# Performance work log

Hardware: AMD Instinct MI355X
Metric: run time of the kernel (lower is better)

The kernel has to match this reference:

```python
import jax, jax.numpy as jnp
import numpy as np

DIM = 768
NUM_HEADS = 12
HEAD_DIM = DIM // NUM_HEADS
SCALE = HEAD_DIM ** -0.5


def setup_inputs() -> dict:
    key = jax.random.key(0)
    k_x, k_qkv, k_pw, k_pb = jax.random.split(key, 4)
    B, N = 2, 4096
    x = jax.random.normal(k_x, (B, N, DIM), dtype=jnp.float32)
    # Linear weights stored as [in, out] for x @ W
    w_qkv = jax.random.normal(k_qkv, (DIM, 3 * DIM), dtype=jnp.float32) * (DIM ** -0.5)
    w_proj = jax.random.normal(k_pw, (DIM, DIM), dtype=jnp.float32) * (DIM ** -0.5)
    b_proj = jax.random.normal(k_pb, (DIM,), dtype=jnp.float32) * 0.02
    return {"x": x, "w_qkv": w_qkv, "w_proj": w_proj, "b_proj": b_proj}


def reference(x, w_qkv, w_proj, b_proj):
    B, N, D = x.shape
    H, Hd = NUM_HEADS, HEAD_DIM
    qkv = (x @ w_qkv).reshape(B, N, 3, H, Hd)
    qkv = jnp.transpose(qkv, (2, 0, 3, 1, 4))  # [3, B, H, N, Hd]
    q, k, v = qkv[0], qkv[1], qkv[2]
    attn = jnp.einsum("bhnd,bhmd->bhnm", q, k) * SCALE  # [B,H,N,N]
    attn = jax.nn.softmax(attn, axis=-1)
    out = jnp.einsum("bhnm,bhmd->bhnd", attn, v)  # [B,H,N,Hd]
    out = jnp.transpose(out, (0, 2, 1, 3)).reshape(B, N, D)
    return out @ w_proj + b_proj
```

## Files before the change

kernel.cpp:

```cpp
#include <hip/hip_runtime.h>
#include <hip/hip_bf16.h>


#define NSEQ 4096
#define NTOK 8192
#define NHD  12
#define QSCALE 0.18033688011112043f

typedef __attribute__((ext_vector_type(8))) __bf16 bf16x8;
typedef __attribute__((ext_vector_type(4))) __bf16 bf16x4;
typedef __attribute__((ext_vector_type(8))) unsigned short u16x8;
typedef __attribute__((ext_vector_type(4))) float  f32x4;

typedef const __attribute__((address_space(1))) unsigned int* as1_u32p;
typedef __attribute__((address_space(3))) unsigned int*       as3_u32p;

#if defined(__has_builtin)
#  if __has_builtin(__builtin_amdgcn_exp2f)
#    define EXP2(x) __builtin_amdgcn_exp2f(x)
#  else
#    define EXP2(x) exp2f(x)
#  endif
#else
#  define EXP2(x) exp2f(x)
#endif

__device__ inline f32x4 mfma16(bf16x8 a, bf16x8 b, f32x4 c) {
    return __builtin_amdgcn_mfma_f32_16x16x32_bf16(a, b, c, 0, 0, 0);
}

__device__ __forceinline__ void gload16(const __bf16* g, __bf16* l) {
    __builtin_amdgcn_global_load_lds((as1_u32p)g, (as3_u32p)l, 16, 0, 0);
}

__global__ __launch_bounds__(256)
void cvt_bf16_kernel(const float* __restrict__ x, __bf16* __restrict__ y)
{
    const size_t i = ((size_t)blockIdx.x * 256 + threadIdx.x) * 8;
    f32x4 a = *(const f32x4*)(x + i);
    f32x4 b = *(const f32x4*)(x + i + 4);
    bf16x8 w;
    #pragma unroll
    for (int j = 0; j < 4; ++j) { w[j] = (__bf16)a[j]; w[4 + j] = (__bf16)b[j]; }
    *(bf16x8*)(y + i) = w;
}

__global__ __launch_bounds__(256)
void wT_kernel(const float* __restrict__ W, __bf16* __restrict__ WT, int K, int N)
{
    __shared__ float t[32][33];
    const int tid = threadIdx.x;
    const int bk = blockIdx.x * 32, bn = blockIdx.y * 32;
    const int tx = tid & 31, ty = tid >> 5;
    #pragma unroll
    for (int i = 0; i < 4; ++i)
        t[ty + 8 * i][tx] = W[(size_t)(bk + ty + 8 * i) * N + bn + tx];
    __syncthreads();
    const int n = bn + (tid >> 3), kc = (tid & 7) * 4;
    bf16x4 w;
    #pragma unroll
    for (int j = 0; j < 4; ++j) w[j] = (__bf16)t[kc + j][tid >> 3];
    *(bf16x4*)(WT + (size_t)n * K + bk + kc) = w;
}

template<int EPI>
__global__ __launch_bounds__(256)
void gemm_kernel(const __bf16* __restrict__ A, const __bf16* __restrict__ BT,
                 const float* __restrict__ bias, void* __restrict__ Cp,
                 int M, int N, int K)
{
    __shared__ __bf16 lds_a[128 * 32];
    __shared__ __bf16 lds_b[128 * 32];
    const int tid  = threadIdx.x;
    const int lane = tid & 63, wave = tid >> 6;
    const int l16  = lane & 15, lg = lane >> 4;
    const int wr = (wave >> 1) * 64, wc = (wave & 1) * 64;
    const int m0 = blockIdx.x * 128, n0 = blockIdx.y * 128;

    f32x4 acc[4][4] = {};

    for (int k0 = 0; k0 < K; k0 += 32) {
        #pragma unroll
        for (int i = 0; i < 2; ++i) {
            const int s   = i * 256 + tid;
            const int row = s >> 2, ch = s & 3;
            __bf16* la = lds_a + (i * 256 + wave * 64) * 8;
            __bf16* lb = lds_b + (i * 256 + wave * 64) * 8;
            gload16(A  + (size_t)(m0 + row) * K + k0 + ch * 8, la);
            gload16(BT + (size_t)(n0 + row) * K + k0 + ch * 8, lb);
        }
        __syncthreads();

        bf16x8 a[4], b[4];
        #pragma unroll
        for (int mf = 0; mf < 4; ++mf)
            a[mf] = *(const bf16x8*)&lds_a[(wr + mf * 16 + l16) * 32 + lg * 8];
        #pragma unroll
        for (int nf = 0; nf < 4; ++nf)
            b[nf] = *(const bf16x8*)&lds_b[(wc + nf * 16 + l16) * 32 + lg * 8];
        __builtin_amdgcn_s_setprio(1);
        #pragma unroll
        for (int mf = 0; mf < 4; ++mf)
            #pragma unroll
            for (int nf = 0; nf < 4; ++nf)
                acc[mf][nf] = mfma16(a[mf], b[nf], acc[mf][nf]);
        __builtin_amdgcn_s_setprio(0);
        __syncthreads();
    }

    #pragma unroll
    for (int mf = 0; mf < 4; ++mf) {
        #pragma unroll
        for (int nf = 0; nf < 4; ++nf) {
            int n = n0 + wc + nf * 16 + l16;
            #pragma unroll
            for (int r = 0; r < 4; ++r) {
                int m = m0 + wr + mf * 16 + lg * 4 + r;
                float v = acc[mf][nf][r];
                if constexpr (EPI == 0) {
                    if (n < 768) v *= QSCALE;
                    ((__bf16*)Cp)[(size_t)m * N + n] = (__bf16)v;
                } else {
                    ((float*)Cp)[(size_t)m * N + n] = v + bias[n];
                }
            }
        }
    }
}

__global__ __launch_bounds__(256)
void attn_kernel(const __bf16* __restrict__ qkv, __bf16* __restrict__ out)
{
    __shared__ __bf16 k_lds[2][64 * 72];
    __shared__ __bf16 v_lds[2][64 * 64];
    __shared__ __bf16 p_lds[4][32 * 72];

    const int tid = threadIdx.x, lane = tid & 63, wave = tid >> 6;
    const int l16 = lane & 15, lg = lane >> 4;

    int bid = (blockIdx.x & 7) * 96 + (blockIdx.x >> 3);
    const int qt = bid & 31;
    const int h  = (bid >> 5) % NHD;
    const int b  = bid / (32 * NHD);
    const size_t rowbase = (size_t)b * NSEQ;
    const int q0 = qt * 128 + wave * 32;

    bf16x8 qf[2][2];
    #pragma unroll
    for (int mf = 0; mf < 2; ++mf)
        #pragma unroll
        for (int ks = 0; ks < 2; ++ks)
            qf[mf][ks] = *(const bf16x8*)(qkv + (rowbase + q0 + mf * 16 + l16) * 2304
                                              + h * 64 + ks * 32 + lg * 8);

    f32x4 o[4][2] = {};
    float l_r[2] = {0.f, 0.f};

    const int krow = tid >> 3, kq = tid & 7;
    const int vt   = tid >> 3, vq = tid & 7;
    u16x8 kreg0, kreg1, vreg0, vreg1;

    auto load_kv = [&](int kt) {
        const unsigned short* q16 = (const unsigned short*)qkv;
        size_t base = rowbase + (size_t)kt * 64;
        kreg0 = *(const u16x8*)(q16 + (base + krow)        * 2304 + 768  + h * 64 + kq * 8);
        kreg1 = *(const u16x8*)(q16 + (base + krow + 32)   * 2304 + 768  + h * 64 + kq * 8);
        vreg0 = *(const u16x8*)(q16 + (base + 2 * vt)      * 2304 + 1536 + h * 64 + vq * 8);
        vreg1 = *(const u16x8*)(q16 + (base + 2 * vt + 1)  * 2304 + 1536 + h * 64 + vq * 8);
    };
    auto store_kv = [&](int bsel) {
        *(u16x8*)&k_lds[bsel][krow * 72 + kq * 8]        = kreg0;
        *(u16x8*)&k_lds[bsel][(krow + 32) * 72 + kq * 8] = kreg1;
        #pragma unroll
        for (int j = 0; j < 8; ++j) {
            int d = vq * 8 + j;
            int chunk = ((vt >> 2) ^ d ^ (d >> 3)) & 7;
            unsigned int val = (unsigned int)vreg0[j] | ((unsigned int)vreg1[j] << 16);
            *(unsigned int*)((char*)&v_lds[bsel][0] + d * 128 + chunk * 16 + (vt & 3) * 4) = val;
        }
    };

    load_kv(0);
    store_kv(0);
    __syncthreads();

    const int NT = NSEQ / 64;
    for (int kt = 0; kt < NT; ++kt) {
        const int cur = kt & 1;
        if (kt + 1 < NT) load_kv(kt + 1);

        f32x4 sc[4][2] = {};
        __builtin_amdgcn_s_setprio(1);
        #pragma unroll
        for (int tf = 0; tf < 4; ++tf) {
            #pragma unroll
            for (int ks = 0; ks < 2; ++ks) {
                bf16x8 kfr = *(const bf16x8*)&k_lds[cur][(tf * 16 + l16) * 72 + ks * 32 + lg * 8];
                #pragma unroll
                for (int mf = 0; mf < 2; ++mf)
                    sc[tf][mf] = mfma16(kfr, qf[mf][ks], sc[tf][mf]);
            }
        }
        __builtin_amdgcn_s_setprio(0);

        #pragma unroll
        for (int mf = 0; mf < 2; ++mf) {
            float rs = 0.f;
            #pragma unroll
            for (int tf = 0; tf < 4; ++tf)
                #pragma unroll
                for (int r = 0; r < 4; ++r) {
                    float p = EXP2(sc[tf][mf][r]);
                    sc[tf][mf][r] = p;
                    rs += p;
                }
            l_r[mf] += rs;
        }

        __bf16* pl = p_lds[wave];
        #pragma unroll
        for (int mf = 0; mf < 2; ++mf)
            #pragma unroll
            for (int tf = 0; tf < 4; ++tf) {
                bf16x4 w;
                #pragma unroll
                for (int r = 0; r < 4; ++r) w[r] = (__bf16)sc[tf][mf][r];
                *(bf16x4*)&pl[(mf * 16 + l16) * 72 + tf * 16 + lg * 4] = w;
            }
    asm volatile("s_waitcnt lgkmcnt(0)" ::: "memory");

        __builtin_amdgcn_s_setprio(1);
        #pragma unroll
        for (int ks = 0; ks < 2; ++ks) {
            bf16x8 pf[2];
            #pragma unroll
            for (int mf = 0; mf < 2; ++mf)
                pf[mf] = *(const bf16x8*)&pl[(mf * 16 + l16) * 72 + ks * 32 + lg * 8];
            #pragma unroll
            for (int nf = 0; nf < 4; ++nf) {
                int d = nf * 16 + l16;
                int chunk = ((ks * 4 + lg) ^ d ^ (d >> 3)) & 7;
                bf16x8 vf = *(const bf16x8*)((const char*)&v_lds[cur][0] + d * 128 + chunk * 16);
                #pragma unroll
                for (int mf = 0; mf < 2; ++mf)
                    o[nf][mf] = mfma16(vf, pf[mf], o[nf][mf]);
            }
        }
        __builtin_amdgcn_s_setprio(0);

        if (kt + 1 < NT) store_kv(cur ^ 1);
        __syncthreads();
    }

    #pragma unroll
    for (int mf = 0; mf < 2; ++mf) {
        l_r[mf] += __shfl_xor(l_r[mf], 16);
        l_r[mf] += __shfl_xor(l_r[mf], 32);
        float inv = 1.0f / l_r[mf];
        size_t row = rowbase + q0 + mf * 16 + l16;
        #pragma unroll
        for (int nf = 0; nf < 4; ++nf) {
            bf16x4 w;
            #pragma unroll
            for (int r = 0; r < 4; ++r) w[r] = (__bf16)(o[nf][mf][r] * inv);
            *(bf16x4*)(out + row * 768 + h * 64 + nf * 16 + lg * 4) = w;
        }
    }
}

extern "C" void kernel_launch(void* const* d_in, const int* in_sizes, int n_in,
                              void* d_out, int out_size, void* d_ws, size_t ws_size,
                              hipStream_t stream)
{
    const float* x      = (const float*)d_in[0];
    const float* w_qkv  = (const float*)d_in[1];
    const float* w_proj = (const float*)d_in[2];
    const float* b_proj = (const float*)d_in[3];
    float* out = (float*)d_out;

    __bf16* qkv    = (__bf16*)d_ws;
    __bf16* attn   = qkv + (size_t)NTOK * 2304;
    __bf16* wqkvT  = attn;
    __bf16* wprojT = attn + (size_t)NTOK * 768;
    __bf16* x_bf16 = (__bf16*)d_out;

    cvt_bf16_kernel<<<dim3(NTOK * 768 / (256 * 8)), 256, 0, stream>>>(x, x_bf16);
    wT_kernel<<<dim3(24, 72), 256, 0, stream>>>(w_qkv, wqkvT, 768, 2304);
    wT_kernel<<<dim3(24, 24), 256, 0, stream>>>(w_proj, wprojT, 768, 768);

    gemm_kernel<0><<<dim3(64, 18), 256, 0, stream>>>(x_bf16, wqkvT, nullptr, qkv,
                                                     NTOK, 3 * 768, 768);
    attn_kernel<<<dim3(2 * NHD * 32), 256, 0, stream>>>(qkv, attn);
    gemm_kernel<1><<<dim3(64, 6), 256, 0, stream>>>(attn, wprojT, b_proj, out,
                                                    NTOK, 768, 768);
}
```

Baseline: 316.5 us.

## Switch attention to 32x32x16 MFMA and keep P in registers via lane shuffles

Rewrites the attention inner loop to use 32x32x16 bf16 MFMA tiles instead of 16x16x32. Because of the new layout, the softmax probabilities can be packed and exchanged across half-waves with shuffles rather than written to and re-read from a per-wave LDS buffer. This removes the P LDS round trip and its wait, and issues fewer, larger MFMA instructions. It also sets an occupancy hint of 3 blocks per CU, which may constrain register allocation.

```diff
diff --git a/kernel.cpp b/kernel.cpp
--- a/kernel.cpp
+++ b/kernel.cpp
@@ -7,10 +7,12 @@
 #define NHD  12
 #define QSCALE 0.18033688011112043f
 
-typedef __attribute__((ext_vector_type(8))) __bf16 bf16x8;
-typedef __attribute__((ext_vector_type(4))) __bf16 bf16x4;
-typedef __attribute__((ext_vector_type(8))) unsigned short u16x8;
-typedef __attribute__((ext_vector_type(4))) float  f32x4;
+typedef __attribute__((ext_vector_type(8)))  __bf16 bf16x8;
+typedef __attribute__((ext_vector_type(4)))  __bf16 bf16x4;
+typedef __attribute__((ext_vector_type(2)))  __bf16 bf16x2;
+typedef __attribute__((ext_vector_type(8)))  unsigned short u16x8;
+typedef __attribute__((ext_vector_type(4)))  float  f32x4;
+typedef __attribute__((ext_vector_type(16))) float  f32x16;
 
 typedef const __attribute__((address_space(1))) unsigned int* as1_u32p;
 typedef __attribute__((address_space(3))) unsigned int*       as3_u32p;
@@ -28,6 +30,15 @@
 __device__ inline f32x4 mfma16(bf16x8 a, bf16x8 b, f32x4 c) {
     return __builtin_amdgcn_mfma_f32_16x16x32_bf16(a, b, c, 0, 0, 0);
 }
+__device__ inline f32x16 mfma32(bf16x8 a, bf16x8 b, f32x16 c) {
+    return __builtin_amdgcn_mfma_f32_32x32x16_bf16(a, b, c, 0, 0, 0);
+}
+
+__device__ inline unsigned int pack2(float x, float y) {
+    union { bf16x2 v; unsigned int u; } c;
+    c.v[0] = (__bf16)x; c.v[1] = (__bf16)y;
+    return c.u;
+}
 
 __device__ __forceinline__ void gload16(const __bf16* g, __bf16* l) {
     __builtin_amdgcn_global_load_lds((as1_u32p)g, (as3_u32p)l, 16, 0, 0);
@@ -128,33 +139,30 @@
     }
 }
 
-__global__ __launch_bounds__(256)
+__global__ __launch_bounds__(256, 3)
 void attn_kernel(const __bf16* __restrict__ qkv, __bf16* __restrict__ out)
 {
     __shared__ __bf16 k_lds[2][64 * 72];
     __shared__ __bf16 v_lds[2][64 * 64];
-    __shared__ __bf16 p_lds[4][32 * 72];
 
     const int tid = threadIdx.x, lane = tid & 63, wave = tid >> 6;
-    const int l16 = lane & 15, lg = lane >> 4;
+    const int l31 = lane & 31, hi = lane >> 5;
+    const bool hib = (hi != 0);
 
     int bid = (blockIdx.x & 7) * 96 + (blockIdx.x >> 3);
     const int qt = bid & 31;
     const int h  = (bid >> 5) % NHD;
     const int b  = bid / (32 * NHD);
     const size_t rowbase = (size_t)b * NSEQ;
-    const int q0 = qt * 128 + wave * 32;
-
-    bf16x8 qf[2][2];
-    #pragma unroll
-    for (int mf = 0; mf < 2; ++mf)
-        #pragma unroll
-        for (int ks = 0; ks < 2; ++ks)
-            qf[mf][ks] = *(const bf16x8*)(qkv + (rowbase + q0 + mf * 16 + l16) * 2304
-                                              + h * 64 + ks * 32 + lg * 8);
-
-    f32x4 o[4][2] = {};
-    float l_r[2] = {0.f, 0.f};
+    const int q = qt * 128 + wave * 32 + l31;
+
+    bf16x8 qf[4];
+    #pragma unroll
+    for (int ks = 0; ks < 4; ++ks)
+        qf[ks] = *(const bf16x8*)(qkv + (rowbase + q) * 2304 + h * 64 + ks * 16 + hi * 8);
+
+    f32x16 o[2] = {};
+    float l_r = 0.f;
 
     const int krow = tid >> 3, kq = tid & 7;
     const int vt   = tid >> 3, vq = tid & 7;
@@ -163,10 +171,10 @@
     auto load_kv = [&](int kt) {
         const unsigned short* q16 = (const unsigned short*)qkv;
         size_t base = rowbase + (size_t)kt * 64;
-        kreg0 = *(const u16x8*)(q16 + (base + krow)        * 2304 + 768  + h * 64 + kq * 8);
-        kreg1 = *(const u16x8*)(q16 + (base + krow + 32)   * 2304 + 768  + h * 64 + kq * 8);
-        vreg0 = *(const u16x8*)(q16 + (base + 2 * vt)      * 2304 + 1536 + h * 64 + vq * 8);
-        vreg1 = *(const u16x8*)(q16 + (base + 2 * vt + 1)  * 2304 + 1536 + h * 64 + vq * 8);
+        kreg0 = *(const u16x8*)(q16 + (base + krow)       * 2304 + 768  + h * 64 + kq * 8);
+        kreg1 = *(const u16x8*)(q16 + (base + krow + 32)  * 2304 + 768  + h * 64 + kq * 8);
+        vreg0 = *(const u16x8*)(q16 + (base + 2 * vt)     * 2304 + 1536 + h * 64 + vq * 8);
+        vreg1 = *(const u16x8*)(q16 + (base + 2 * vt + 1) * 2304 + 1536 + h * 64 + vq * 8);
     };
     auto store_kv = [&](int bsel) {
         *(u16x8*)&k_lds[bsel][krow * 72 + kq * 8]        = kreg0;
@@ -189,61 +197,56 @@
         const int cur = kt & 1;
         if (kt + 1 < NT) load_kv(kt + 1);
 
-        f32x4 sc[4][2] = {};
+        f32x16 sc[2] = {};
         __builtin_amdgcn_s_setprio(1);
         #pragma unroll
-        for (int tf = 0; tf < 4; ++tf) {
-            #pragma unroll
-            for (int ks = 0; ks < 2; ++ks) {
-                bf16x8 kfr = *(const bf16x8*)&k_lds[cur][(tf * 16 + l16) * 72 + ks * 32 + lg * 8];
-                #pragma unroll
-                for (int mf = 0; mf < 2; ++mf)
-                    sc[tf][mf] = mfma16(kfr, qf[mf][ks], sc[tf][mf]);
+        for (int tb = 0; tb < 2; ++tb) {
+            #pragma unroll
+            for (int ks = 0; ks < 4; ++ks) {
+                bf16x8 kf = *(const bf16x8*)&k_lds[cur][(tb * 32 + l31) * 72 + ks * 16 + hi * 8];
+                sc[tb] = mfma32(kf, qf[ks], sc[tb]);
             }
         }
         __builtin_amdgcn_s_setprio(0);
 
-        #pragma unroll
-        for (int mf = 0; mf < 2; ++mf) {
-            float rs = 0.f;
-            #pragma unroll
-            for (int tf = 0; tf < 4; ++tf)
-                #pragma unroll
-                for (int r = 0; r < 4; ++r) {
-                    float p = EXP2(sc[tf][mf][r]);
-                    sc[tf][mf][r] = p;
-                    rs += p;
-                }
-            l_r[mf] += rs;
-        }
-
-        __bf16* pl = p_lds[wave];
-        #pragma unroll
-        for (int mf = 0; mf < 2; ++mf)
-            #pragma unroll
-            for (int tf = 0; tf < 4; ++tf) {
-                bf16x4 w;
-                #pragma unroll
-                for (int r = 0; r < 4; ++r) w[r] = (__bf16)sc[tf][mf][r];
-                *(bf16x4*)&pl[(mf * 16 + l16) * 72 + tf * 16 + lg * 4] = w;
-            }
-    asm volatile("s_waitcnt lgkmcnt(0)" ::: "memory");
+        unsigned int pk0[2][4], pk1[2][4];
+        float rs = 0.f;
+        #pragma unroll
+        for (int tb = 0; tb < 2; ++tb) {
+            #pragma unroll
+            for (int g = 0; g < 4; ++g) {
+                float p0 = EXP2(sc[tb][4 * g + 0]);
+                float p1 = EXP2(sc[tb][4 * g + 1]);
+                float p2 = EXP2(sc[tb][4 * g + 2]);
+                float p3 = EXP2(sc[tb][4 * g + 3]);
+                rs += (p0 + p1) + (p2 + p3);
+                pk0[tb][g] = pack2(p0, p1);
+                pk1[tb][g] = pack2(p2, p3);
+            }
+        }
+        l_r += rs;
 
         __builtin_amdgcn_s_setprio(1);
         #pragma unroll
-        for (int ks = 0; ks < 2; ++ks) {
-            bf16x8 pf[2];
-            #pragma unroll
-            for (int mf = 0; mf < 2; ++mf)
-                pf[mf] = *(const bf16x8*)&pl[(mf * 16 + l16) * 72 + ks * 32 + lg * 8];
-            #pragma unroll
-            for (int nf = 0; nf < 4; ++nf) {
-                int d = nf * 16 + l16;
-                int chunk = ((ks * 4 + lg) ^ d ^ (d >> 3)) & 7;
+        for (int ks = 0; ks < 4; ++ks) {
+            const int tb = ks >> 1, gL = 2 * (ks & 1), gH = gL + 1;
+            unsigned int pL0 = pk0[tb][gL], pL1 = pk1[tb][gL];
+            unsigned int pH0 = pk0[tb][gH], pH1 = pk1[tb][gH];
+            unsigned int rL0 = (unsigned int)__shfl_xor((int)pL0, 32);
+            unsigned int rL1 = (unsigned int)__shfl_xor((int)pL1, 32);
+            unsigned int rH0 = (unsigned int)__shfl_xor((int)pH0, 32);
+            unsigned int rH1 = (unsigned int)__shfl_xor((int)pH1, 32);
+            union { bf16x8 v; unsigned int u[4]; } pf;
+            pf.u[0] = hib ? rH0 : pL0;
+            pf.u[1] = hib ? rH1 : pL1;
+            pf.u[2] = hib ? pH0 : rL0;
+            pf.u[3] = hib ? pH1 : rL1;
+            #pragma unroll
+            for (int db = 0; db < 2; ++db) {
+                int d = db * 32 + l31;
+                int chunk = ((2 * ks + hi) ^ d ^ (d >> 3)) & 7;
                 bf16x8 vf = *(const bf16x8*)((const char*)&v_lds[cur][0] + d * 128 + chunk * 16);
-                #pragma unroll
-                for (int mf = 0; mf < 2; ++mf)
-                    o[nf][mf] = mfma16(vf, pf[mf], o[nf][mf]);
+                o[db] = mfma32(vf, pf.v, o[db]);
             }
         }
         __builtin_amdgcn_s_setprio(0);
@@ -252,18 +255,18 @@
         __syncthreads();
     }
 
-    #pragma unroll
-    for (int mf = 0; mf < 2; ++mf) {
-        l_r[mf] += __shfl_xor(l_r[mf], 16);
-        l_r[mf] += __shfl_xor(l_r[mf], 32);
-        float inv = 1.0f / l_r[mf];
-        size_t row = rowbase + q0 + mf * 16 + l16;
-        #pragma unroll
-        for (int nf = 0; nf < 4; ++nf) {
+    l_r += __shfl_xor(l_r, 32);
+    float inv = 1.0f / l_r;
+    size_t row = rowbase + q;
+    #pragma unroll
+    for (int db = 0; db < 2; ++db) {
+        #pragma unroll
+        for (int rr = 0; rr < 4; ++rr) {
+            int d0 = db * 32 + rr * 8 + hi * 4;
             bf16x4 w;
             #pragma unroll
-            for (int r = 0; r < 4; ++r) w[r] = (__bf16)(o[nf][mf][r] * inv);
-            *(bf16x4*)(out + row * 768 + h * 64 + nf * 16 + lg * 4) = w;
+            for (int i = 0; i < 4; ++i) w[i] = (__bf16)(o[db][4 * rr + i] * inv);
+            *(bf16x4*)(out + row * 768 + h * 64 + d0) = w;
         }
     }
 }
```

Result: faster. 286.5 us (-9.5%).
